# Optimization experiments

Measured on AMD Instinct MI355X. Metric: run time of the kernel, lower is better.

## Reference

```python
import jax, jax.numpy as jnp
import numpy as np

N_HEAD = 16
OUTPUT_DIM = 1024
HEAD_DIM = OUTPUT_DIM // N_HEAD  # 64


def setup_inputs() -> dict:
    key = jax.random.key(0)
    kq, kk, kv = jax.random.split(key, 3)
    B, S, D = 4, 2048, OUTPUT_DIM
    return {
        "Q": jax.random.normal(kq, (B, S, D), dtype=jnp.float32),
        "K": jax.random.normal(kk, (B, S, D), dtype=jnp.float32),
        "V": jax.random.normal(kv, (B, S, D), dtype=jnp.float32),
    }


def reference(Q, K, V):
    # FAITHFUL to the original Keras layer: it reshapes Q into K and V as well
    # (K = reshape(Q, ...), V = reshape(Q, ...)), so the K and V inputs are
    # ignored and attention is computed of Q against itself.
    B, S, _ = Q.shape
    q = Q.reshape(B, S, N_HEAD, HEAD_DIM)  # [B,S,H,D]
    scale = 1.0 / np.sqrt(HEAD_DIM).astype(np.float32)
    # scores: [B,H,S,S]
    scores = jnp.einsum("bshd,bthd->bhst", q, q) * scale
    attn = jax.nn.softmax(scores, axis=-1)
    out = jnp.einsum("bhst,bthd->bshd", attn, q)  # [B,S,H,D]
    # concat of per-head slices along last axis == head-major reshape
    return out.reshape(B, S, N_HEAD * HEAD_DIM)
```

## Files before the change

### kernel.cpp

```cpp
#include <hip/hip_runtime.h>
#include <stdint.h>

#define S_LEN 2048
#define DH    64
#define NH    16
#define DM    1024
#define NBH   64

typedef float    f32x4 __attribute__((ext_vector_type(4)));
typedef _Float16 half8 __attribute__((ext_vector_type(8)));
typedef _Float16 half4 __attribute__((ext_vector_type(4)));

__global__ __launch_bounds__(256, 4) void attn_v6_kernel(const float* __restrict__ Q,
                                                         float* __restrict__ out) {
    __shared__ __align__(16) _Float16 KnS[64 * 64];
    __shared__ __align__(16) _Float16 KtS[64 * 64];
    __shared__ __align__(16) _Float16 Pb[4][32 * 64];

    const int tid  = threadIdx.x;
    const int w    = tid >> 6;
    const int lane = tid & 63;
    const int quad = lane >> 4;
    const int l15  = lane & 15;
    const int xq   = l15 & 7;

    const int bid     = blockIdx.x;
    const int logical = (bid & 7) * 128 + (bid >> 3);
    const int qblk    = logical & 15;
    const int bh      = logical >> 4;
    const int b = bh >> 4, h = bh & 15;
    const int q0      = qblk * 128 + w * 32;

    const float* qbase = Q + (size_t)b * S_LEN * DM + h * DH;

    half8 qreg[2][2];
    #pragma unroll
    for (int nch = 0; nch < 2; ++nch) {
        const float* p = qbase + (size_t)(q0 + nch * 16 + l15) * DM + quad * 8;
        #pragma unroll
        for (int s = 0; s < 2; ++s) {
            const float4 f0 = *(const float4*)(p + s * 32);
            const float4 f1 = *(const float4*)(p + s * 32 + 4);
            qreg[nch][s] = (half8){ (_Float16)f0.x, (_Float16)f0.y, (_Float16)f0.z, (_Float16)f0.w,
                                    (_Float16)f1.x, (_Float16)f1.y, (_Float16)f1.z, (_Float16)f1.w };
        }
    }

    const float qs = 0.18033688011112042f;
    float m_c[2];
    #pragma unroll
    for (int nch = 0; nch < 2; ++nch) {
        float part = 0.f;
        #pragma unroll
        for (int s = 0; s < 2; ++s)
            #pragma unroll
            for (int j = 0; j < 8; ++j) { const float x = (float)qreg[nch][s][j]; part += x * x; }
        part += __shfl_xor(part, 16, 64);
        part += __shfl_xor(part, 32, 64);
        m_c[nch] = qs * part;
    }

    const int rA = tid >> 2;
    const int c4 = tid & 3;
    const float* srcA = qbase + (size_t)rA * DM + c4 * 4;
    _Float16* knA[4];
    #pragma unroll
    for (int j = 0; j < 4; ++j) {
        const int chunk = 2 * j + (c4 >> 1);
        knA[j] = &KnS[rA * 64 + ((chunk ^ (rA & 7)) * 8) + (c4 & 1) * 4];
    }
    const int kj0 = (tid & 15) * 4;
    const int d0b = (tid >> 4) * 4;
    const float* srcB = qbase + (size_t)kj0 * DM + d0b;
    _Float16* ktB[4];
    #pragma unroll
    for (int dd = 0; dd < 4; ++dd) {
        const int dr = d0b + dd;
        ktB[dd] = &KtS[dr * 64 + (((kj0 >> 3) ^ (dr & 7)) * 8) + (kj0 & 7)];
    }

    f32x4 O[2][4];
    #pragma unroll
    for (int m = 0; m < 2; ++m)
        #pragma unroll
        for (int n = 0; n < 4; ++n) O[m][n] = (f32x4){0.f, 0.f, 0.f, 0.f};
    float lsum[2] = {0.f, 0.f};
    _Float16* Pw = Pb[w];

    for (int tt = 0; tt < S_LEN / 64; ++tt) {
        __syncthreads();

        float4 av[4];
        #pragma unroll
        for (int j = 0; j < 4; ++j)
            av[j] = *(const float4*)(srcA + (size_t)(tt * 64) * DM + j * 16);
        float4 bv[4];
        #pragma unroll
        for (int i = 0; i < 4; ++i)
            bv[i] = *(const float4*)(srcB + (size_t)(tt * 64 + i) * DM);

        #pragma unroll
        for (int j = 0; j < 4; ++j) {
            const half4 ha = (half4){ (_Float16)av[j].x, (_Float16)av[j].y,
                                      (_Float16)av[j].z, (_Float16)av[j].w };
            *(half4*)knA[j] = ha;
        }
        half4 hb[4];
        #pragma unroll
        for (int i = 0; i < 4; ++i)
            hb[i] = (half4){ (_Float16)bv[i].x, (_Float16)bv[i].y,
                             (_Float16)bv[i].z, (_Float16)bv[i].w };
        #pragma unroll
        for (int dd = 0; dd < 4; ++dd) {
            const half4 tv = (half4){ hb[0][dd], hb[1][dd], hb[2][dd], hb[3][dd] };
            *(half4*)ktB[dd] = tv;
        }
        __syncthreads();

        #pragma unroll
        for (int mch = 0; mch < 4; ++mch) {
            const half8 a0 = *(const half8*)&KnS[(mch * 16 + l15) * 64 + ((quad ^ xq) * 8)];
            const half8 a1 = *(const half8*)&KnS[(mch * 16 + l15) * 64 + (((4 + quad) ^ xq) * 8)];
            const int wc   = 2 * mch + (quad >> 1);
            const int woff = (quad & 1) * 4;
            #pragma unroll
            for (int nch = 0; nch < 2; ++nch) {
                f32x4 acc = (f32x4){0.f, 0.f, 0.f, 0.f};
                acc = __builtin_amdgcn_mfma_f32_16x16x32_f16(a0, qreg[nch][0], acc, 0, 0, 0);
                acc = __builtin_amdgcn_mfma_f32_16x16x32_f16(a1, qreg[nch][1], acc, 0, 0, 0);
                const float p0 = __builtin_amdgcn_exp2f(__builtin_fmaf(acc[0], qs, -m_c[nch]));
                const float p1 = __builtin_amdgcn_exp2f(__builtin_fmaf(acc[1], qs, -m_c[nch]));
                const float p2 = __builtin_amdgcn_exp2f(__builtin_fmaf(acc[2], qs, -m_c[nch]));
                const float p3 = __builtin_amdgcn_exp2f(__builtin_fmaf(acc[3], qs, -m_c[nch]));
                lsum[nch] += (p0 + p1) + (p2 + p3);
                const half4 hvp = (half4){ (_Float16)p0, (_Float16)p1, (_Float16)p2, (_Float16)p3 };
                *(half4*)&Pw[(nch * 16 + l15) * 64 + ((wc ^ xq) * 8) + woff] = hvp;
            }
        }

        half8 pf[2][2];
        #pragma unroll
        for (int qb = 0; qb < 2; ++qb) {
            pf[qb][0] = *(const half8*)&Pw[(qb * 16 + l15) * 64 + ((quad ^ xq) * 8)];
            pf[qb][1] = *(const half8*)&Pw[(qb * 16 + l15) * 64 + (((4 + quad) ^ xq) * 8)];
        }
        #pragma unroll
        for (int nch = 0; nch < 4; ++nch) {
            const half8 v0 = *(const half8*)&KtS[(nch * 16 + l15) * 64 + ((quad ^ xq) * 8)];
            const half8 v1 = *(const half8*)&KtS[(nch * 16 + l15) * 64 + (((4 + quad) ^ xq) * 8)];
            #pragma unroll
            for (int qb = 0; qb < 2; ++qb) {
                O[qb][nch] = __builtin_amdgcn_mfma_f32_16x16x32_f16(pf[qb][0], v0, O[qb][nch], 0, 0, 0);
                O[qb][nch] = __builtin_amdgcn_mfma_f32_16x16x32_f16(pf[qb][1], v1, O[qb][nch], 0, 0, 0);
            }
        }
    }

    float lcol[2];
    #pragma unroll
    for (int qb = 0; qb < 2; ++qb) {
        float l = lsum[qb];
        l += __shfl_xor(l, 16, 64);
        l += __shfl_xor(l, 32, 64);
        lcol[qb] = l;
    }
    float* ob = out + (size_t)b * S_LEN * DM + h * DH;
    #pragma unroll
    for (int qb = 0; qb < 2; ++qb) {
        float inv[4];
        #pragma unroll
        for (int r = 0; r < 4; ++r)
            inv[r] = 1.0f / __shfl(lcol[qb], quad * 4 + r, 16);
        #pragma unroll
        for (int nch = 0; nch < 4; ++nch)
            #pragma unroll
            for (int r = 0; r < 4; ++r)
                ob[(size_t)(q0 + qb * 16 + quad * 4 + r) * DM + nch * 16 + l15] = O[qb][nch][r] * inv[r];
    }
}

extern "C" void kernel_launch(void* const* d_in, const int* in_sizes, int n_in,
                              void* d_out, int out_size, void* d_ws, size_t ws_size,
                              hipStream_t stream) {
    const float* Q = (const float*)d_in[0];
    float* out = (float*)d_out;
    (void)d_ws; (void)ws_size;
    attn_v6_kernel<<<dim3(NBH * (S_LEN / 128)), dim3(256), 0, stream>>>(Q, out);
}
```

Baseline: 209.8 us.

## Switch attention to 32x32x16 MFMA with register-resident P via permlane32 swap

Replaces the 16x16x32 MFMA tiling with 32x32x16 MFMAs for both the QK^T and PV products. The probability tile is converted with packed RTZ conversions and rearranged across lane halves with v_permlane32_swap, so it goes straight into the PV MFMA A-operand. This removes the per-wave LDS P buffer and its write/read round trip and lowers MFMA instruction count. The costs are larger accumulators (two f32x16 outputs plus a 16-wide score accumulator), the dropped launch_bounds hint, possible occupancy loss, and reliance on gfx950-specific inline asm.

```diff
diff --git a/kernel.cpp b/kernel.cpp
--- a/kernel.cpp
+++ b/kernel.cpp
@@ -6,23 +6,24 @@
 #define NH    16
 #define DM    1024
 #define NBH   64
+#define NT    (S_LEN / 64)
 
-typedef float    f32x4 __attribute__((ext_vector_type(4)));
-typedef _Float16 half8 __attribute__((ext_vector_type(8)));
-typedef _Float16 half4 __attribute__((ext_vector_type(4)));
+typedef float    f32x16 __attribute__((ext_vector_type(16)));
+typedef float    f32x4  __attribute__((ext_vector_type(4)));
+typedef _Float16 half8  __attribute__((ext_vector_type(8)));
+typedef _Float16 half4  __attribute__((ext_vector_type(4)));
+typedef _Float16 half2v __attribute__((ext_vector_type(2)));
 
-__global__ __launch_bounds__(256, 4) void attn_v6_kernel(const float* __restrict__ Q,
-                                                         float* __restrict__ out) {
+__global__ void attn_v10_kernel(const float* __restrict__ Q,
+                                float* __restrict__ out) {
     __shared__ __align__(16) _Float16 KnS[64 * 64];
     __shared__ __align__(16) _Float16 KtS[64 * 64];
-    __shared__ __align__(16) _Float16 Pb[4][32 * 64];
 
     const int tid  = threadIdx.x;
     const int w    = tid >> 6;
     const int lane = tid & 63;
-    const int quad = lane >> 4;
-    const int l15  = lane & 15;
-    const int xq   = l15 & 7;
+    const int l31  = lane & 31;
+    const int hi   = lane >> 5;
 
     const int bid     = blockIdx.x;
     const int logical = (bid & 7) * 128 + (bid >> 3);
@@ -33,32 +34,24 @@
 
     const float* qbase = Q + (size_t)b * S_LEN * DM + h * DH;
 
-    half8 qreg[2][2];
+    half8 qreg[4];
     #pragma unroll
-    for (int nch = 0; nch < 2; ++nch) {
-        const float* p = qbase + (size_t)(q0 + nch * 16 + l15) * DM + quad * 8;
-        #pragma unroll
-        for (int s = 0; s < 2; ++s) {
-            const float4 f0 = *(const float4*)(p + s * 32);
-            const float4 f1 = *(const float4*)(p + s * 32 + 4);
-            qreg[nch][s] = (half8){ (_Float16)f0.x, (_Float16)f0.y, (_Float16)f0.z, (_Float16)f0.w,
-                                    (_Float16)f1.x, (_Float16)f1.y, (_Float16)f1.z, (_Float16)f1.w };
-        }
+    for (int s = 0; s < 4; ++s) {
+        const float* p = qbase + (size_t)(q0 + l31) * DM + s * 16 + hi * 8;
+        const float4 f0 = *(const float4*)p;
+        const float4 f1 = *(const float4*)(p + 4);
+        qreg[s] = (half8){ (_Float16)f0.x, (_Float16)f0.y, (_Float16)f0.z, (_Float16)f0.w,
+                           (_Float16)f1.x, (_Float16)f1.y, (_Float16)f1.z, (_Float16)f1.w };
     }
 
     const float qs = 0.18033688011112042f;
-    float m_c[2];
+    float part = 0.f;
     #pragma unroll
-    for (int nch = 0; nch < 2; ++nch) {
-        float part = 0.f;
+    for (int s = 0; s < 4; ++s)
         #pragma unroll
-        for (int s = 0; s < 2; ++s)
-            #pragma unroll
-            for (int j = 0; j < 8; ++j) { const float x = (float)qreg[nch][s][j]; part += x * x; }
-        part += __shfl_xor(part, 16, 64);
-        part += __shfl_xor(part, 32, 64);
-        m_c[nch] = qs * part;
-    }
+        for (int j = 0; j < 8; ++j) { const float x = (float)qreg[s][j]; part += x * x; }
+    part += __shfl_xor(part, 32, 64);
+    const float m_c = qs * part;
 
     const int rA = tid >> 2;
     const int c4 = tid & 3;
@@ -79,15 +72,11 @@
         ktB[dd] = &KtS[dr * 64 + (((kj0 >> 3) ^ (dr & 7)) * 8) + (kj0 & 7)];
     }
 
-    f32x4 O[2][4];
-    #pragma unroll
-    for (int m = 0; m < 2; ++m)
-        #pragma unroll
-        for (int n = 0; n < 4; ++n) O[m][n] = (f32x4){0.f, 0.f, 0.f, 0.f};
-    float lsum[2] = {0.f, 0.f};
-    _Float16* Pw = Pb[w];
+    f32x16 O0 = { 0.f,0.f,0.f,0.f, 0.f,0.f,0.f,0.f, 0.f,0.f,0.f,0.f, 0.f,0.f,0.f,0.f };
+    f32x16 O1 = { 0.f,0.f,0.f,0.f, 0.f,0.f,0.f,0.f, 0.f,0.f,0.f,0.f, 0.f,0.f,0.f,0.f };
+    float lsum = 0.f;
 
-    for (int tt = 0; tt < S_LEN / 64; ++tt) {
+    for (int tt = 0; tt < NT; ++tt) {
         __syncthreads();
 
         float4 av[4];
@@ -118,64 +107,63 @@
         __syncthreads();
 
         #pragma unroll
-        for (int mch = 0; mch < 4; ++mch) {
-            const half8 a0 = *(const half8*)&KnS[(mch * 16 + l15) * 64 + ((quad ^ xq) * 8)];
-            const half8 a1 = *(const half8*)&KnS[(mch * 16 + l15) * 64 + (((4 + quad) ^ xq) * 8)];
-            const int wc   = 2 * mch + (quad >> 1);
-            const int woff = (quad & 1) * 4;
+        for (int kt = 0; kt < 2; ++kt) {
+            f32x16 acc = { 0.f,0.f,0.f,0.f, 0.f,0.f,0.f,0.f,
+                           0.f,0.f,0.f,0.f, 0.f,0.f,0.f,0.f };
             #pragma unroll
-            for (int nch = 0; nch < 2; ++nch) {
-                f32x4 acc = (f32x4){0.f, 0.f, 0.f, 0.f};
-                acc = __builtin_amdgcn_mfma_f32_16x16x32_f16(a0, qreg[nch][0], acc, 0, 0, 0);
-                acc = __builtin_amdgcn_mfma_f32_16x16x32_f16(a1, qreg[nch][1], acc, 0, 0, 0);
-                const float p0 = __builtin_amdgcn_exp2f(__builtin_fmaf(acc[0], qs, -m_c[nch]));
-                const float p1 = __builtin_amdgcn_exp2f(__builtin_fmaf(acc[1], qs, -m_c[nch]));
-                const float p2 = __builtin_amdgcn_exp2f(__builtin_fmaf(acc[2], qs, -m_c[nch]));
-                const float p3 = __builtin_amdgcn_exp2f(__builtin_fmaf(acc[3], qs, -m_c[nch]));
-                lsum[nch] += (p0 + p1) + (p2 + p3);
-                const half4 hvp = (half4){ (_Float16)p0, (_Float16)p1, (_Float16)p2, (_Float16)p3 };
-                *(half4*)&Pw[(nch * 16 + l15) * 64 + ((wc ^ xq) * 8) + woff] = hvp;
+            for (int s = 0; s < 4; ++s) {
+                const half8 a = *(const half8*)&KnS[(kt * 32 + l31) * 64 +
+                                                    (((2 * s + hi) ^ (l31 & 7)) * 8)];
+                acc = __builtin_amdgcn_mfma_f32_32x32x16_f16(a, qreg[s], acc, 0, 0, 0);
             }
-        }
-
-        half8 pf[2][2];
-        #pragma unroll
-        for (int qb = 0; qb < 2; ++qb) {
-            pf[qb][0] = *(const half8*)&Pw[(qb * 16 + l15) * 64 + ((quad ^ xq) * 8)];
-            pf[qb][1] = *(const half8*)&Pw[(qb * 16 + l15) * 64 + (((4 + quad) ^ xq) * 8)];
-        }
-        #pragma unroll
-        for (int nch = 0; nch < 4; ++nch) {
-            const half8 v0 = *(const half8*)&KtS[(nch * 16 + l15) * 64 + ((quad ^ xq) * 8)];
-            const half8 v1 = *(const half8*)&KtS[(nch * 16 + l15) * 64 + (((4 + quad) ^ xq) * 8)];
+            float p[16];
             #pragma unroll
-            for (int qb = 0; qb < 2; ++qb) {
-                O[qb][nch] = __builtin_amdgcn_mfma_f32_16x16x32_f16(pf[qb][0], v0, O[qb][nch], 0, 0, 0);
-                O[qb][nch] = __builtin_amdgcn_mfma_f32_16x16x32_f16(pf[qb][1], v1, O[qb][nch], 0, 0, 0);
+            for (int r = 0; r < 16; ++r) {
+                p[r] = __builtin_amdgcn_exp2f(__builtin_fmaf(acc[r], qs, -m_c));
+                lsum += p[r];
+            }
+            half2v d0 = __builtin_bit_cast(half2v, __builtin_amdgcn_cvt_pkrtz(p[0],  p[1]));
+            half2v d1 = __builtin_bit_cast(half2v, __builtin_amdgcn_cvt_pkrtz(p[2],  p[3]));
+            half2v d2 = __builtin_bit_cast(half2v, __builtin_amdgcn_cvt_pkrtz(p[4],  p[5]));
+            half2v d3 = __builtin_bit_cast(half2v, __builtin_amdgcn_cvt_pkrtz(p[6],  p[7]));
+            half2v d4 = __builtin_bit_cast(half2v, __builtin_amdgcn_cvt_pkrtz(p[8],  p[9]));
+            half2v d5 = __builtin_bit_cast(half2v, __builtin_amdgcn_cvt_pkrtz(p[10], p[11]));
+            half2v d6 = __builtin_bit_cast(half2v, __builtin_amdgcn_cvt_pkrtz(p[12], p[13]));
+            half2v d7 = __builtin_bit_cast(half2v, __builtin_amdgcn_cvt_pkrtz(p[14], p[15]));
+            asm volatile("v_permlane32_swap_b32 %0, %1" : "+v"(d0), "+v"(d2));
+            asm volatile("v_permlane32_swap_b32 %0, %1" : "+v"(d1), "+v"(d3));
+            asm volatile("v_permlane32_swap_b32 %0, %1" : "+v"(d4), "+v"(d6));
+            asm volatile("v_permlane32_swap_b32 %0, %1" : "+v"(d5), "+v"(d7));
+            const half8 pa0 = (half8){ d0[0], d0[1], d1[0], d1[1],
+                                       d2[0], d2[1], d3[0], d3[1] };
+            const half8 pa1 = (half8){ d4[0], d4[1], d5[0], d5[1],
+                                       d6[0], d6[1], d7[0], d7[1] };
+            {
+                const int sg0 = 2 * kt;
+                const half8 b00 = *(const half8*)&KtS[(0 * 32 + l31) * 64 +
+                                                      (((2 * sg0 + hi) ^ (l31 & 7)) * 8)];
+                const half8 b01 = *(const half8*)&KtS[(0 * 32 + l31) * 64 +
+                                                      (((2 * sg0 + 2 + hi) ^ (l31 & 7)) * 8)];
+                O0 = __builtin_amdgcn_mfma_f32_32x32x16_f16(pa0, b00, O0, 0, 0, 0);
+                O0 = __builtin_amdgcn_mfma_f32_32x32x16_f16(pa1, b01, O0, 0, 0, 0);
+                const half8 b10 = *(const half8*)&KtS[(1 * 32 + l31) * 64 +
+                                                      (((2 * sg0 + hi) ^ (l31 & 7)) * 8)];
+                const half8 b11 = *(const half8*)&KtS[(1 * 32 + l31) * 64 +
+                                                      (((2 * sg0 + 2 + hi) ^ (l31 & 7)) * 8)];
+                O1 = __builtin_amdgcn_mfma_f32_32x32x16_f16(pa0, b10, O1, 0, 0, 0);
+                O1 = __builtin_amdgcn_mfma_f32_32x32x16_f16(pa1, b11, O1, 0, 0, 0);
             }
         }
     }
 
-    float lcol[2];
-    #pragma unroll
-    for (int qb = 0; qb < 2; ++qb) {
-        float l = lsum[qb];
-        l += __shfl_xor(l, 16, 64);
-        l += __shfl_xor(l, 32, 64);
-        lcol[qb] = l;
-    }
+    const float lt = lsum + __shfl_xor(lsum, 32, 64);
     float* ob = out + (size_t)b * S_LEN * DM + h * DH;
     #pragma unroll
-    for (int qb = 0; qb < 2; ++qb) {
-        float inv[4];
-        #pragma unroll
-        for (int r = 0; r < 4; ++r)
-            inv[r] = 1.0f / __shfl(lcol[qb], quad * 4 + r, 16);
-        #pragma unroll
-        for (int nch = 0; nch < 4; ++nch)
-            #pragma unroll
-            for (int r = 0; r < 4; ++r)
-                ob[(size_t)(q0 + qb * 16 + quad * 4 + r) * DM + nch * 16 + l15] = O[qb][nch][r] * inv[r];
+    for (int r = 0; r < 16; ++r) {
+        const int qr = (r & 3) + 8 * (r >> 2) + 4 * hi;
+        const float inv = 1.0f / __shfl(lt, qr, 64);
+        ob[(size_t)(q0 + qr) * DM + l31]      = O0[r] * inv;
+        ob[(size_t)(q0 + qr) * DM + 32 + l31] = O1[r] * inv;
     }
 }
 
@@ -185,5 +173,5 @@
     const float* Q = (const float*)d_in[0];
     float* out = (float*)d_out;
     (void)d_ws; (void)ws_size;
-    attn_v6_kernel<<<dim3(NBH * (S_LEN / 128)), dim3(256), 0, stream>>>(Q, out);
+    attn_v10_kernel<<<dim3(NBH * (S_LEN / 128)), dim3(256), 0, stream>>>(Q, out);
 }
```

After: 210.0 us. Within noise of the previous version (+0.1%).
